# Optimization experiments

Hardware: AMD Instinct MI355X
Metric: run time of the kernel (lower is better)

## Reference

```python
import jax, jax.numpy as jnp
import numpy as np

L, D, H, KV, HD, KVL, I, PL = 8, 2048, 8, 2, 256, 4096, 8192, 256
FULL = (4,)          # layers with full (global) attention / global RoPE
POS = 2047           # current decode position (cache write slot)
N_REP = H // KV      # GQA expansion factor


def rms(x, eps=1e-6):
    # RMSNorm without scale (v_norm); scale applied by caller where needed
    return x * jax.lax.rsqrt(jnp.mean(x * x, axis=-1, keepdims=True) + eps)


def rope(x, cos, sin):
    half = HD // 2
    rot = jnp.concatenate([-x[..., half:], x[..., :half]], axis=-1)
    return x * cos + rot * sin


def _rope_tables(theta):
    inv = 1.0 / (theta ** (np.arange(0, HD, 2, dtype=np.float32) / HD))
    ang = jnp.asarray(POS * inv, dtype=jnp.float32)
    return jnp.concatenate([jnp.cos(ang)] * 2), jnp.concatenate([jnp.sin(ang)] * 2)


def setup_inputs() -> dict:
    key = jax.random.key(0)
    ks = jax.random.split(key, 24)
    r = lambda k, s, sc=0.02: jax.random.normal(k, s, jnp.float32) * sc
    gains = lambda k, s: 1.0 + jax.random.normal(k, s, jnp.float32) * 0.02
    cos_s, sin_s = _rope_tables(10000.0)
    cos_f, sin_f = _rope_tables(1000000.0)
    um = jnp.zeros((1, 1, KVL, 1), jnp.float32).at[0, 0, POS, 0].set(1.0)
    mask = jnp.where(jnp.arange(KVL) <= POS, 0.0, -1e9).astype(jnp.float32)
    return {
        "hidden_states": r(ks[0], (1, 1, D), 1.0),
        "causal_mask": mask,
        "update_mask": um,
        "per_layer_combined": r(ks[1], (1, 1, L * PL), 1.0),
        "cos_s": cos_s, "sin_s": sin_s, "cos_f": cos_f, "sin_f": sin_f,
        "K_in": r(ks[2], (L, KV, KVL, HD)),
        "V_in": r(ks[3], (L, KV, KVL, HD)),
        "w_q": r(ks[4], (L, H * HD, D)),
        "w_k": r(ks[5], (L, KV * HD, D)),
        "w_v": r(ks[6], (L, KV * HD, D)),
        "w_o": r(ks[7], (L, D, H * HD)),
        "g_in_ln": gains(ks[8], (L, D)),
        "g_q_norm": gains(ks[9], (L, HD)),
        "g_k_norm": gains(ks[10], (L, HD)),
        "g_post_attn_ln": gains(ks[11], (L, D)),
        "g_pre_ff_ln": gains(ks[12], (L, D)),
        "g_post_ff_ln": gains(ks[13], (L, D)),
        "w_gate": r(ks[14], (L, I, D)),
        "w_up": r(ks[15], (L, I, D)),
        "w_down": r(ks[16], (L, D, I)),
        "w_plg": r(ks[17], (L, PL, D)),
        "w_plp": r(ks[18], (L, D, PL)),
        "g_post_pl_ln": gains(ks[19], (L, D)),
        "layer_scalar": jnp.ones((L,), jnp.float32),
    }


def reference(hidden_states, causal_mask, update_mask, per_layer_combined,
              cos_s, sin_s, cos_f, sin_f, K_in, V_in,
              w_q, w_k, w_v, w_o,
              g_in_ln, g_q_norm, g_k_norm, g_post_attn_ln, g_pre_ff_ln, g_post_ff_ln,
              w_gate, w_up, w_down, w_plg, w_plp, g_post_pl_ln, layer_scalar):
    um = update_mask[0, 0]          # [KVL,1] one-hot at write position
    h = hidden_states[0, 0]         # [D], batch=1/seq=1 decode
    K_outs, V_outs = [], []
    for i in range(L):
        cos, sin = (cos_f, sin_f) if i in FULL else (cos_s, sin_s)
        # --- attention block ---
        res = h
        x = rms(h) * g_in_ln[i]
        q = rms((w_q[i] @ x).reshape(H, HD)) * g_q_norm[i]
        q = rope(q, cos, sin)                                   # [H,HD]
        k = rms((w_k[i] @ x).reshape(KV, HD)) * g_k_norm[i]
        k = rope(k, cos, sin)                                   # [KV,HD]
        v = rms((w_v[i] @ x).reshape(KV, HD))                    # v_norm (no scale)
        # full-tensor masked blend = KV cache write (faithful to source)
        Ko = K_in[i] * (1.0 - um) + k[:, None, :] * um          # [KV,KVL,HD]
        Vo = V_in[i] * (1.0 - um) + v[:, None, :] * um
        K_outs.append(Ko); V_outs.append(Vo)
        Ke = jnp.repeat(Ko, N_REP, axis=0)                      # GQA expand [H,KVL,HD]
        Ve = jnp.repeat(Vo, N_REP, axis=0)
        scores = jnp.einsum('hd,hkd->hk', q, Ke) + causal_mask  # no 1/sqrt(hd) in source
        attn = jax.nn.softmax(scores, axis=-1)
        ao = jnp.einsum('hk,hkd->hd', attn, Ve).reshape(H * HD)
        ao = rms(w_o[i] @ ao) * g_post_attn_ln[i]
        h = res + ao
        # --- gated MLP ---
        res = h
        xm = rms(h) * g_pre_ff_ln[i]
        m = w_down[i] @ (jax.nn.gelu(w_gate[i] @ xm, approximate=True) * (w_up[i] @ xm))
        h = res + rms(m) * g_post_ff_ln[i]
        # --- per-layer input gating ---
        res = h
        pls = per_layer_combined[0, 0, i * PL:(i + 1) * PL]     # [PL]
        g = jax.nn.gelu(w_plg[i] @ h, approximate=True) * pls
        h = res + rms(w_plp[i] @ g) * g_post_pl_ln[i]
        h = h * layer_scalar[i]
    return (h[None, None, :], jnp.stack(K_outs), jnp.stack(V_outs))
```

## Files before the change

kernel.cpp:

```cpp
#include <hip/hip_runtime.h>

#define NL   8
#define DIM  2048
#define NH   8
#define NKV  2
#define HD   256
#define KVL  4096
#define FFI  8192
#define PLD  256
#define POS  2047
#define NCH  16
#define CP   128

__device__ __forceinline__ float dot4(float4 a, float4 b){
  return a.x*b.x + a.y*b.y + a.z*b.z + a.w*b.w;
}

__device__ __forceinline__ float waveAllSum(float v){
#pragma unroll
  for(int o=1;o<64;o<<=1) v += __shfl_xor(v,o,64);
  return v;
}

__device__ __forceinline__ float waveAllMax(float v){
#pragma unroll
  for(int o=1;o<64;o<<=1) v = fmaxf(v, __shfl_xor(v,o,64));
  return v;
}

__device__ __forceinline__ float blockSum256(float v, float* red){
  int lane = threadIdx.x & 63, w = threadIdx.x >> 6;
  v = waveAllSum(v);
  __syncthreads();
  if(lane==0) red[w] = v;
  __syncthreads();
  return red[0]+red[1]+red[2]+red[3];
}

__device__ __forceinline__ float gelu_tanh(float v){
  return 0.5f*v*(1.0f + tanhf(0.7978845608028654f*(v + 0.044715f*v*v*v)));
}

__global__ __launch_bounds__(256) void qkv_k(
    const float* __restrict__ Wq, const float* __restrict__ Wk,
    const float* __restrict__ Wv,
    const float* __restrict__ hC, const float* __restrict__ u,
    const float* __restrict__ g_pl, const float* __restrict__ lsc,
    const float* __restrict__ g_in, const float* __restrict__ hidden,
    float* __restrict__ hA, float* __restrict__ qkv){
  __shared__ float xs[DIM];
  __shared__ float red[4];
  int tid = threadIdx.x;
  float hv[8];
  if(hidden){
#pragma unroll
    for(int i=0;i<8;i++) hv[i] = hidden[tid + i*256];
  } else {
    float uv[8]; float ss1 = 0.f;
#pragma unroll
    for(int i=0;i<8;i++){ uv[i] = u[tid + i*256]; ss1 += uv[i]*uv[i]; }
    ss1 = blockSum256(ss1, red);
    float r1 = rsqrtf(ss1*(1.f/DIM) + 1e-6f);
    float ls = lsc[0];
#pragma unroll
    for(int i=0;i<8;i++){
      int idx = tid + i*256;
      hv[i] = (hC[idx] + uv[i]*r1*g_pl[idx])*ls;
    }
  }
  float ss2 = 0.f;
#pragma unroll
  for(int i=0;i<8;i++) ss2 += hv[i]*hv[i];
  ss2 = blockSum256(ss2, red);
  float r2 = rsqrtf(ss2*(1.f/DIM) + 1e-6f);
#pragma unroll
  for(int i=0;i<8;i++){
    int idx = tid + i*256;
    xs[idx] = hv[i]*r2*g_in[idx];
    if(blockIdx.x==0) hA[idx] = hv[i];
  }
  __syncthreads();
  int lane = tid & 63, wv = tid >> 6;
  int r = blockIdx.x*4 + wv;
  const float* W; int row;
  if(r < 2048){ W = Wq; row = r; }
  else if(r < 2560){ W = Wk; row = r - 2048; }
  else { W = Wv; row = r - 2560; }
  const float4* Wr = (const float4*)(W + (size_t)row*DIM);
  const float4* xs4 = (const float4*)xs;
  float acc = 0.f;
#pragma unroll
  for(int i=0;i<DIM/256;i++) acc += dot4(Wr[lane + i*64], xs4[lane + i*64]);
  acc = waveAllSum(acc);
  if(lane==0) qkv[r] = acc;
}

__device__ __forceinline__ float4 normRope(const float* __restrict__ raw, int lane,
    const float* __restrict__ gain, const float* __restrict__ cosT,
    const float* __restrict__ sinT, bool doRope){
  float4 v4 = ((const float4*)raw)[lane];
  float ss = waveAllSum(dot4(v4,v4));
  float sc = rsqrtf(ss*(1.f/HD) + 1e-6f);
  float4 n;
  if(gain){
    float4 g4 = ((const float4*)gain)[lane];
    n.x=v4.x*sc*g4.x; n.y=v4.y*sc*g4.y; n.z=v4.z*sc*g4.z; n.w=v4.w*sc*g4.w;
  } else {
    n.x=v4.x*sc; n.y=v4.y*sc; n.z=v4.z*sc; n.w=v4.w*sc;
  }
  if(!doRope) return n;
  float4 np;
  np.x=__shfl_xor(n.x,32,64); np.y=__shfl_xor(n.y,32,64);
  np.z=__shfl_xor(n.z,32,64); np.w=__shfl_xor(n.w,32,64);
  float4 c4 = ((const float4*)cosT)[lane];
  float4 s4 = ((const float4*)sinT)[lane];
  float sg = (lane < 32) ? -1.f : 1.f;
  float4 o;
  o.x = n.x*c4.x + sg*np.x*s4.x;
  o.y = n.y*c4.y + sg*np.y*s4.y;
  o.z = n.z*c4.z + sg*np.z*s4.z;
  o.w = n.w*c4.w + sg*np.w*s4.w;
  return o;
}

__global__ __launch_bounds__(256) void attn_k(
    const float* __restrict__ qkv,
    const float* __restrict__ gq, const float* __restrict__ gk,
    const float* __restrict__ cosT, const float* __restrict__ sinT,
    float* __restrict__ Kc, float* __restrict__ Vc,
    float* __restrict__ pm, float* __restrict__ pl, float* __restrict__ po){
  int b = blockIdx.x;
  int tid = threadIdx.x, lane = tid & 63, wv = tid >> 6;

  if(b == NKV*NCH){
    int kvv = wv >> 1, isV = wv & 1;
    const float* raw = qkv + (isV ? 2560 : 2048) + kvv*HD;
    float4 o = normRope(raw, lane, isV ? nullptr : gk, cosT, sinT, !isV);
    float* dst = (isV ? Vc : Kc) + ((size_t)kvv*KVL + POS)*HD;
    ((float4*)dst)[lane] = o;
    return;
  }

  int kv = b >> 4, c = b & (NCH-1);
  __shared__ float q_s[4][HD];
  __shared__ float kf[HD], vf[HD];
  __shared__ float s_s[4][CP];
  __shared__ float s_w[4][CP];

  {
    float4 o = normRope(qkv + (kv*4 + wv)*HD, lane, gq, cosT, sinT, true);
    ((float4*)q_s[wv])[lane] = o;
  }
  bool fresh = (c == NCH-1);
  if(fresh){
    if(wv == 0){
      float4 o = normRope(qkv + 2048 + kv*HD, lane, gk, cosT, sinT, true);
      ((float4*)kf)[lane] = o;
    } else if(wv == 1){
      float4 o = normRope(qkv + 2560 + kv*HD, lane, nullptr, cosT, sinT, false);
      ((float4*)vf)[lane] = o;
    }
  }
  __syncthreads();

  float4 q4[4];
#pragma unroll
  for(int hh=0;hh<4;hh++) q4[hh] = ((const float4*)q_s[hh])[lane];
  const float4* Kp = (const float4*)(Kc + ((size_t)kv*KVL + c*CP)*HD);
  for(int j=0;j<CP/4;j++){
    int p = wv*(CP/4) + j;
    float4 k4 = (fresh && p==CP-1) ? ((const float4*)kf)[lane]
                                   : Kp[(size_t)p*64 + lane];
    float d0 = dot4(k4,q4[0]), d1 = dot4(k4,q4[1]);
    float d2 = dot4(k4,q4[2]), d3 = dot4(k4,q4[3]);
    d0 = waveAllSum(d0); d1 = waveAllSum(d1);
    d2 = waveAllSum(d2); d3 = waveAllSum(d3);
    if(lane==0){ s_s[0][p]=d0; s_s[1][p]=d1; s_s[2][p]=d2; s_s[3][p]=d3; }
  }
  __syncthreads();

  {
    float s0 = s_s[wv][lane], s1 = s_s[wv][lane+64];
    float m = waveAllMax(fmaxf(s0,s1));
    float e0 = __expf(s0-m), e1 = __expf(s1-m);
    s_w[wv][lane] = e0; s_w[wv][lane+64] = e1;
    float lsum = waveAllSum(e0+e1);
    if(lane==0){
      int hg = kv*4 + wv;
      pm[hg*NCH + c] = m;
      pl[hg*NCH + c] = lsum;
    }
  }
  __syncthreads();

  float acc[4] = {0.f,0.f,0.f,0.f};
  const float* Vp = Vc + ((size_t)kv*KVL + c*CP)*HD;
  for(int p=0;p<CP;p++){
    float vv = (fresh && p==CP-1) ? vf[tid] : Vp[(size_t)p*HD + tid];
#pragma unroll
    for(int hh=0;hh<4;hh++) acc[hh] += s_w[hh][p]*vv;
  }
#pragma unroll
  for(int hh=0;hh<4;hh++){
    int hg = kv*4 + hh;
    po[((size_t)hg*NCH + c)*HD + tid] = acc[hh];
  }
}

__global__ __launch_bounds__(256) void wo_k(const float* __restrict__ W,
    const float* __restrict__ pm, const float* __restrict__ pl,
    const float* __restrict__ po, float* __restrict__ y){
  __shared__ float ao_s[DIM];
  __shared__ float se_s[NH][NCH];
  __shared__ float Ms[NH];
  __shared__ float Li[NH];
  int tid = threadIdx.x;
  if(tid < NH){
    float m = -1e30f;
    for(int c=0;c<NCH;c++) m = fmaxf(m, pm[tid*NCH+c]);
    Ms[tid] = m;
  }
  __syncthreads();
  if(tid < NH*NCH){
    int h = tid >> 4, c = tid & (NCH-1);
    se_s[h][c] = __expf(pm[h*NCH+c] - Ms[h]);
  }
  __syncthreads();
  if(tid < NH){
    float L = 0.f;
    for(int c=0;c<NCH;c++) L += pl[tid*NCH+c]*se_s[tid][c];
    Li[tid] = 1.f/L;
  }
  __syncthreads();
  for(int h=0;h<NH;h++){
    float a = 0.f;
#pragma unroll
    for(int c=0;c<NCH;c++) a += po[((size_t)h*NCH+c)*HD + tid]*se_s[h][c];
    ao_s[h*HD + tid] = a*Li[h];
  }
  __syncthreads();
  int lane = tid & 63, wv = tid >> 6;
  int r = blockIdx.x*4 + wv;
  const float4* Wr = (const float4*)(W + (size_t)r*DIM);
  const float4* xs4 = (const float4*)ao_s;
  float acc = 0.f;
#pragma unroll
  for(int i=0;i<DIM/256;i++) acc += dot4(Wr[lane + i*64], xs4[lane + i*64]);
  acc = waveAllSum(acc);
  if(lane==0) y[r] = acc;
}

__global__ __launch_bounds__(256) void gateup_k(const float* __restrict__ Wg,
    const float* __restrict__ Wu, const float* __restrict__ y,
    const float* __restrict__ hA, const float* __restrict__ g_pa,
    const float* __restrict__ g_pf, float* __restrict__ hB, float* __restrict__ t){
  __shared__ float xs[DIM];
  __shared__ float red[4];
  int tid = threadIdx.x;
  float yv[8]; float ss1 = 0.f;
#pragma unroll
  for(int i=0;i<8;i++){ yv[i] = y[tid + i*256]; ss1 += yv[i]*yv[i]; }
  ss1 = blockSum256(ss1, red);
  float r1 = rsqrtf(ss1*(1.f/DIM) + 1e-6f);
  float hv[8]; float ss2 = 0.f;
#pragma unroll
  for(int i=0;i<8;i++){
    int idx = tid + i*256;
    hv[i] = hA[idx] + yv[i]*r1*g_pa[idx];
    ss2 += hv[i]*hv[i];
  }
  ss2 = blockSum256(ss2, red);
  float r2 = rsqrtf(ss2*(1.f/DIM) + 1e-6f);
#pragma unroll
  for(int i=0;i<8;i++){
    int idx = tid + i*256;
    xs[idx] = hv[i]*r2*g_pf[idx];
    if(blockIdx.x==0) hB[idx] = hv[i];
  }
  __syncthreads();
  int lane = tid & 63, wv = tid >> 6;
  int j = blockIdx.x*4 + wv;
  const float4* Gr = (const float4*)(Wg + (size_t)j*DIM);
  const float4* Ur = (const float4*)(Wu + (size_t)j*DIM);
  const float4* xs4 = (const float4*)xs;
  float ag = 0.f, au = 0.f;
#pragma unroll
  for(int i=0;i<DIM/256;i++){
    float4 bv = xs4[lane + i*64];
    ag += dot4(Gr[lane + i*64], bv);
    au += dot4(Ur[lane + i*64], bv);
  }
  ag = waveAllSum(ag);
  au = waveAllSum(au);
  if(lane==0) t[j] = gelu_tanh(ag)*au;
}

template<int C>
__global__ __launch_bounds__(256) void gemv_k(const float* __restrict__ W,
    const float* __restrict__ x, float* __restrict__ y){
  __shared__ float xs[C];
  for(int i=threadIdx.x; i<C/4; i+=256)
    ((float4*)xs)[i] = ((const float4*)x)[i];
  __syncthreads();
  int lane = threadIdx.x & 63, wv = threadIdx.x >> 6;
  int r = blockIdx.x*4 + wv;
  const float4* Wr = (const float4*)(W + (size_t)r*C);
  const float4* xs4 = (const float4*)xs;
  float acc = 0.f;
#pragma unroll
  for(int i=0;i<C/256;i++) acc += dot4(Wr[lane + i*64], xs4[lane + i*64]);
  acc = waveAllSum(acc);
  if(lane==0) y[r] = acc;
}

__global__ __launch_bounds__(256) void plg_k(const float* __restrict__ W,
    const float* __restrict__ mv, const float* __restrict__ hB,
    const float* __restrict__ g_ff, const float* __restrict__ pls,
    float* __restrict__ hCout, float* __restrict__ gb){
  __shared__ float xs[DIM];
  __shared__ float red[4];
  int tid = threadIdx.x;
  float mvv[8]; float ss1 = 0.f;
#pragma unroll
  for(int i=0;i<8;i++){ mvv[i] = mv[tid + i*256]; ss1 += mvv[i]*mvv[i]; }
  ss1 = blockSum256(ss1, red);
  float r1 = rsqrtf(ss1*(1.f/DIM) + 1e-6f);
#pragma unroll
  for(int i=0;i<8;i++){
    int idx = tid + i*256;
    float hc = hB[idx] + mvv[i]*r1*g_ff[idx];
    xs[idx] = hc;
    if(blockIdx.x==0) hCout[idx] = hc;
  }
  __syncthreads();
  int lane = tid & 63, wv = tid >> 6;
  int r = blockIdx.x*4 + wv;
  const float4* Wr = (const float4*)(W + (size_t)r*DIM);
  const float4* xs4 = (const float4*)xs;
  float acc = 0.f;
#pragma unroll
  for(int i=0;i<DIM/256;i++) acc += dot4(Wr[lane + i*64], xs4[lane + i*64]);
  acc = waveAllSum(acc);
  if(lane==0) gb[r] = gelu_tanh(acc)*pls[r];
}

__global__ __launch_bounds__(256) void final_k(const float* __restrict__ u,
    const float* __restrict__ hC, const float* __restrict__ g_pl,
    const float* __restrict__ lsc, float* __restrict__ out){
  __shared__ float red[4];
  int tid = threadIdx.x;
  float uv[8]; float ss1 = 0.f;
#pragma unroll
  for(int i=0;i<8;i++){ uv[i] = u[tid + i*256]; ss1 += uv[i]*uv[i]; }
  ss1 = blockSum256(ss1, red);
  float r1 = rsqrtf(ss1*(1.f/DIM) + 1e-6f);
  float ls = lsc[0];
#pragma unroll
  for(int i=0;i<8;i++){
    int idx = tid + i*256;
    out[idx] = (hC[idx] + uv[i]*r1*g_pl[idx])*ls;
  }
}

extern "C" void kernel_launch(void* const* d_in, const int* in_sizes, int n_in,
                              void* d_out, int out_size, void* d_ws, size_t ws_size,
                              hipStream_t stream){
  const float* hidden   = (const float*)d_in[0];
  const float* plc      = (const float*)d_in[3];
  const float* cos_s    = (const float*)d_in[4];
  const float* sin_s    = (const float*)d_in[5];
  const float* cos_f    = (const float*)d_in[6];
  const float* sin_f    = (const float*)d_in[7];
  const float* K_in     = (const float*)d_in[8];
  const float* V_in     = (const float*)d_in[9];
  const float* w_q      = (const float*)d_in[10];
  const float* w_k      = (const float*)d_in[11];
  const float* w_v      = (const float*)d_in[12];
  const float* w_o      = (const float*)d_in[13];
  const float* g_in_ln  = (const float*)d_in[14];
  const float* g_q_norm = (const float*)d_in[15];
  const float* g_k_norm = (const float*)d_in[16];
  const float* g_pa_ln  = (const float*)d_in[17];
  const float* g_pf_ln  = (const float*)d_in[18];
  const float* g_ff_ln  = (const float*)d_in[19];
  const float* w_gate   = (const float*)d_in[20];
  const float* w_up     = (const float*)d_in[21];
  const float* w_down   = (const float*)d_in[22];
  const float* w_plg    = (const float*)d_in[23];
  const float* w_plp    = (const float*)d_in[24];
  const float* g_pl_ln  = (const float*)d_in[25];
  const float* l_scal   = (const float*)d_in[26];

  float* out  = (float*)d_out;
  float* outK = out + DIM;
  float* outV = outK + (size_t)NL*NKV*KVL*HD;

  float* ws   = (float*)d_ws;
  float* hA   = ws;
  float* hB   = ws + 2048;
  float* hC   = ws + 4096;
  float* qkv  = ws + 6144;
  float* y    = ws + 9216;
  float* t    = ws + 11264;
  float* mv   = ws + 19456;
  float* gb   = ws + 21504;
  float* u    = ws + 21760;
  float* pm   = ws + 23808;
  float* pl   = ws + 23936;
  float* po   = ws + 24064;

  (void)hipMemcpyAsync(outK, K_in, (size_t)NL*NKV*KVL*HD*sizeof(float),
                       hipMemcpyDeviceToDevice, stream);
  (void)hipMemcpyAsync(outV, V_in, (size_t)NL*NKV*KVL*HD*sizeof(float),
                       hipMemcpyDeviceToDevice, stream);

  for(int l=0;l<NL;l++){
    const float* cosT = (l==4) ? cos_f : cos_s;
    const float* sinT = (l==4) ? sin_f : sin_s;
    float* Kl = outK + (size_t)l*NKV*KVL*HD;
    float* Vl = outV + (size_t)l*NKV*KVL*HD;

    qkv_k<<<768,256,0,stream>>>(
        w_q + (size_t)l*NH*HD*DIM, w_k + (size_t)l*NKV*HD*DIM,
        w_v + (size_t)l*NKV*HD*DIM,
        hC, u,
        (l>0) ? g_pl_ln + (size_t)(l-1)*DIM : g_pl_ln,
        (l>0) ? l_scal + (l-1) : l_scal,
        g_in_ln + (size_t)l*DIM,
        (l==0) ? hidden : nullptr,
        hA, qkv);

    attn_k<<<NKV*NCH+1,256,0,stream>>>(qkv, g_q_norm + l*HD, g_k_norm + l*HD,
                                       cosT, sinT, Kl, Vl, pm, pl, po);

    wo_k<<<512,256,0,stream>>>(w_o + (size_t)l*DIM*NH*HD, pm, pl, po, y);

    gateup_k<<<FFI/4,256,0,stream>>>(w_gate + (size_t)l*FFI*DIM,
                                     w_up + (size_t)l*FFI*DIM,
                                     y, hA, g_pa_ln + (size_t)l*DIM,
                                     g_pf_ln + (size_t)l*DIM, hB, t);

    gemv_k<FFI><<<512,256,0,stream>>>(w_down + (size_t)l*DIM*FFI, t, mv);

    plg_k<<<PLD/4,256,0,stream>>>(w_plg + (size_t)l*PLD*DIM, mv, hB,
                                  g_ff_ln + (size_t)l*DIM, plc + l*PLD, hC, gb);

    gemv_k<PLD><<<512,256,0,stream>>>(w_plp + (size_t)l*DIM*PLD, gb, u);
  }

  final_k<<<1,256,0,stream>>>(u, hC, g_pl_ln + (size_t)(NL-1)*DIM,
                              l_scal + (NL-1), out);
}
```

Before: 976.5 us.

## Replace per-layer kernel launches with persistent megakernel using grid barriers

Merges all per-layer kernels into one persistent kernel of 256 blocks × 512 threads, with a software grid barrier between stages. This removes roughly 57 kernel launches and their inter-kernel gaps. The KV cache copy moves from two large hipMemcpyAsync calls into the QKV stage, spread across all waves. Attention is split into 256 chunks of 8 positions with a two-level softmax merge. The design relies on all 256 blocks being co-resident and adds barrier spin costs and lower per-stage parallelism.

```diff
diff --git a/kernel.cpp b/kernel.cpp
--- a/kernel.cpp
+++ b/kernel.cpp
@@ -9,8 +9,22 @@
 #define FFI  8192
 #define PLD  256
 #define POS  2047
-#define NCH  16
-#define CP   128
+#define NCH  256
+#define CP   8
+#define NBLK 256
+#define NTHR 512
+
+struct MegaP {
+  const float *hidden, *plc, *cos_s, *sin_s, *cos_f, *sin_f;
+  const float *K_in, *V_in;
+  const float *w_q, *w_k, *w_v, *w_o;
+  const float *g_in, *g_q, *g_k, *g_pa, *g_pf, *g_ff;
+  const float *w_gate, *w_up, *w_down, *w_plg, *w_plp, *g_pl, *lsc;
+  float *out, *outK, *outV;
+  float *hA, *hB, *hC, *qkvb, *y, *t, *mv, *gb, *u;
+  float *pm, *pl, *po, *po2, *Mq, *Lq;
+  unsigned *slots, *gen;
+};
 
 __device__ __forceinline__ float dot4(float4 a, float4 b){
   return a.x*b.x + a.y*b.y + a.z*b.z + a.w*b.w;
@@ -28,71 +42,20 @@
   return v;
 }
 
-__device__ __forceinline__ float blockSum256(float v, float* red){
+__device__ __forceinline__ float blockSum512(float v, float* red){
   int lane = threadIdx.x & 63, w = threadIdx.x >> 6;
   v = waveAllSum(v);
   __syncthreads();
   if(lane==0) red[w] = v;
   __syncthreads();
-  return red[0]+red[1]+red[2]+red[3];
+  float s = 0.f;
+#pragma unroll
+  for(int i=0;i<8;i++) s += red[i];
+  return s;
 }
 
 __device__ __forceinline__ float gelu_tanh(float v){
   return 0.5f*v*(1.0f + tanhf(0.7978845608028654f*(v + 0.044715f*v*v*v)));
-}
-
-__global__ __launch_bounds__(256) void qkv_k(
-    const float* __restrict__ Wq, const float* __restrict__ Wk,
-    const float* __restrict__ Wv,
-    const float* __restrict__ hC, const float* __restrict__ u,
-    const float* __restrict__ g_pl, const float* __restrict__ lsc,
-    const float* __restrict__ g_in, const float* __restrict__ hidden,
-    float* __restrict__ hA, float* __restrict__ qkv){
-  __shared__ float xs[DIM];
-  __shared__ float red[4];
-  int tid = threadIdx.x;
-  float hv[8];
-  if(hidden){
-#pragma unroll
-    for(int i=0;i<8;i++) hv[i] = hidden[tid + i*256];
-  } else {
-    float uv[8]; float ss1 = 0.f;
-#pragma unroll
-    for(int i=0;i<8;i++){ uv[i] = u[tid + i*256]; ss1 += uv[i]*uv[i]; }
-    ss1 = blockSum256(ss1, red);
-    float r1 = rsqrtf(ss1*(1.f/DIM) + 1e-6f);
-    float ls = lsc[0];
-#pragma unroll
-    for(int i=0;i<8;i++){
-      int idx = tid + i*256;
-      hv[i] = (hC[idx] + uv[i]*r1*g_pl[idx])*ls;
-    }
-  }
-  float ss2 = 0.f;
-#pragma unroll
-  for(int i=0;i<8;i++) ss2 += hv[i]*hv[i];
-  ss2 = blockSum256(ss2, red);
-  float r2 = rsqrtf(ss2*(1.f/DIM) + 1e-6f);
-#pragma unroll
-  for(int i=0;i<8;i++){
-    int idx = tid + i*256;
-    xs[idx] = hv[i]*r2*g_in[idx];
-    if(blockIdx.x==0) hA[idx] = hv[i];
-  }
-  __syncthreads();
-  int lane = tid & 63, wv = tid >> 6;
-  int r = blockIdx.x*4 + wv;
-  const float* W; int row;
-  if(r < 2048){ W = Wq; row = r; }
-  else if(r < 2560){ W = Wk; row = r - 2048; }
-  else { W = Wv; row = r - 2560; }
-  const float4* Wr = (const float4*)(W + (size_t)row*DIM);
-  const float4* xs4 = (const float4*)xs;
-  float acc = 0.f;
-#pragma unroll
-  for(int i=0;i<DIM/256;i++) acc += dot4(Wr[lane + i*64], xs4[lane + i*64]);
-  acc = waveAllSum(acc);
-  if(lane==0) qkv[r] = acc;
 }
 
 __device__ __forceinline__ float4 normRope(const float* __restrict__ raw, int lane,
@@ -123,331 +86,411 @@
   return o;
 }
 
-__global__ __launch_bounds__(256) void attn_k(
-    const float* __restrict__ qkv,
-    const float* __restrict__ gq, const float* __restrict__ gk,
-    const float* __restrict__ cosT, const float* __restrict__ sinT,
-    float* __restrict__ Kc, float* __restrict__ Vc,
-    float* __restrict__ pm, float* __restrict__ pl, float* __restrict__ po){
-  int b = blockIdx.x;
-  int tid = threadIdx.x, lane = tid & 63, wv = tid >> 6;
-
-  if(b == NKV*NCH){
-    int kvv = wv >> 1, isV = wv & 1;
-    const float* raw = qkv + (isV ? 2560 : 2048) + kvv*HD;
-    float4 o = normRope(raw, lane, isV ? nullptr : gk, cosT, sinT, !isV);
-    float* dst = (isV ? Vc : Kc) + ((size_t)kvv*KVL + POS)*HD;
-    ((float4*)dst)[lane] = o;
-    return;
-  }
-
-  int kv = b >> 4, c = b & (NCH-1);
-  __shared__ float q_s[4][HD];
-  __shared__ float kf[HD], vf[HD];
-  __shared__ float s_s[4][CP];
-  __shared__ float s_w[4][CP];
-
-  {
-    float4 o = normRope(qkv + (kv*4 + wv)*HD, lane, gq, cosT, sinT, true);
-    ((float4*)q_s[wv])[lane] = o;
-  }
-  bool fresh = (c == NCH-1);
-  if(fresh){
-    if(wv == 0){
-      float4 o = normRope(qkv + 2048 + kv*HD, lane, gk, cosT, sinT, true);
-      ((float4*)kf)[lane] = o;
-    } else if(wv == 1){
-      float4 o = normRope(qkv + 2560 + kv*HD, lane, nullptr, cosT, sinT, false);
-      ((float4*)vf)[lane] = o;
+__device__ __forceinline__ void gridBarrier(unsigned* slots, unsigned* gen, unsigned g){
+  __syncthreads();
+  int tid = threadIdx.x, bid = blockIdx.x;
+  if(tid < 64){
+    if(tid == 0){
+      __threadfence();
+      __hip_atomic_store(&slots[bid], g, __ATOMIC_RELEASE, __HIP_MEMORY_SCOPE_AGENT);
+    }
+    if(bid == 0){
+      for(;;){
+        bool ok = true;
+#pragma unroll
+        for(int i=0;i<4;i++){
+          unsigned v = __hip_atomic_load(&slots[tid*4+i], __ATOMIC_ACQUIRE,
+                                         __HIP_MEMORY_SCOPE_AGENT);
+          ok &= (v >= g);
+        }
+        if(__all(ok)) break;
+        __builtin_amdgcn_s_sleep(1);
+      }
+      if(tid == 0)
+        __hip_atomic_store(gen, g, __ATOMIC_RELEASE, __HIP_MEMORY_SCOPE_AGENT);
+    } else if(tid == 0){
+      while(__hip_atomic_load(gen, __ATOMIC_ACQUIRE, __HIP_MEMORY_SCOPE_AGENT) < g){
+        __builtin_amdgcn_s_sleep(2);
+      }
     }
   }
   __syncthreads();
-
-  float4 q4[4];
-#pragma unroll
-  for(int hh=0;hh<4;hh++) q4[hh] = ((const float4*)q_s[hh])[lane];
-  const float4* Kp = (const float4*)(Kc + ((size_t)kv*KVL + c*CP)*HD);
-  for(int j=0;j<CP/4;j++){
-    int p = wv*(CP/4) + j;
-    float4 k4 = (fresh && p==CP-1) ? ((const float4*)kf)[lane]
-                                   : Kp[(size_t)p*64 + lane];
-    float d0 = dot4(k4,q4[0]), d1 = dot4(k4,q4[1]);
-    float d2 = dot4(k4,q4[2]), d3 = dot4(k4,q4[3]);
-    d0 = waveAllSum(d0); d1 = waveAllSum(d1);
-    d2 = waveAllSum(d2); d3 = waveAllSum(d3);
-    if(lane==0){ s_s[0][p]=d0; s_s[1][p]=d1; s_s[2][p]=d2; s_s[3][p]=d3; }
+}
+
+__global__ __launch_bounds__(NTHR, 2) void mega_k(MegaP p){
+  __shared__ float xs[FFI];
+  __shared__ float red[8];
+  float4* xs4 = (float4*)xs;
+
+  const int tid  = threadIdx.x;
+  const int bid  = blockIdx.x;
+  const int lane = tid & 63;
+  const int wv   = tid >> 6;
+  const int gw   = bid*8 + wv;
+  unsigned bgen = 0;
+
+  for(int l=0; l<NL; l++){
+    const float* Wq  = p.w_q    + (size_t)l*NH*HD*DIM;
+    const float* Wk  = p.w_k    + (size_t)l*NKV*HD*DIM;
+    const float* Wv  = p.w_v    + (size_t)l*NKV*HD*DIM;
+    const float* Wo  = p.w_o    + (size_t)l*DIM*NH*HD;
+    const float* Wg  = p.w_gate + (size_t)l*FFI*DIM;
+    const float* Wu  = p.w_up   + (size_t)l*FFI*DIM;
+    const float* Wd  = p.w_down + (size_t)l*DIM*FFI;
+    const float* Wpg = p.w_plg  + (size_t)l*PLD*DIM;
+    const float* Wpp = p.w_plp  + (size_t)l*DIM*PLD;
+    const float* cosT = (l==4) ? p.cos_f : p.cos_s;
+    const float* sinT = (l==4) ? p.sin_f : p.sin_s;
+    const float* gq = p.g_q + (size_t)l*HD;
+    const float* gk = p.g_k + (size_t)l*HD;
+    float* Kl = p.outK + (size_t)l*NKV*KVL*HD;
+    float* Vl = p.outV + (size_t)l*NKV*KVL*HD;
+    const float* Ki = p.K_in + (size_t)l*NKV*KVL*HD;
+    const float* Vi = p.V_in + (size_t)l*NKV*KVL*HD;
+
+    {
+      float hv[4];
+      if(l==0){
+#pragma unroll
+        for(int i=0;i<4;i++) hv[i] = p.hidden[tid + i*512];
+      } else {
+        const float* gpl = p.g_pl + (size_t)(l-1)*DIM;
+        float ls = p.lsc[l-1];
+        float uv[4]; float ss = 0.f;
+#pragma unroll
+        for(int i=0;i<4;i++){ uv[i] = p.u[tid + i*512]; ss += uv[i]*uv[i]; }
+        ss = blockSum512(ss, red);
+        float r1 = rsqrtf(ss*(1.f/DIM) + 1e-6f);
+#pragma unroll
+        for(int i=0;i<4;i++){
+          int idx = tid + i*512;
+          hv[i] = (p.hC[idx] + uv[i]*r1*gpl[idx])*ls;
+        }
+      }
+      float ss2 = 0.f;
+#pragma unroll
+      for(int i=0;i<4;i++) ss2 += hv[i]*hv[i];
+      ss2 = blockSum512(ss2, red);
+      float r2 = rsqrtf(ss2*(1.f/DIM) + 1e-6f);
+      const float* gin = p.g_in + (size_t)l*DIM;
+#pragma unroll
+      for(int i=0;i<4;i++){
+        int idx = tid + i*512;
+        xs[idx] = hv[i]*r2*gin[idx];
+        if(bid==0) p.hA[idx] = hv[i];
+      }
+      __syncthreads();
+
+      {
+        const float4* Wr = (const float4*)(Wq + (size_t)gw*DIM);
+        float acc = 0.f;
+#pragma unroll
+        for(int i=0;i<8;i++) acc += dot4(Wr[i*64+lane], xs4[i*64+lane]);
+        acc = waveAllSum(acc);
+        if(lane==0) p.qkvb[gw] = acc;
+      }
+      if(gw < 1024){
+        const float* W; int row;
+        if(gw < 512){ W = Wk; row = gw; } else { W = Wv; row = gw - 512; }
+        const float4* Wr = (const float4*)(W + (size_t)row*DIM);
+        float acc = 0.f;
+#pragma unroll
+        for(int i=0;i<8;i++) acc += dot4(Wr[i*64+lane], xs4[i*64+lane]);
+        acc = waveAllSum(acc);
+        if(lane==0) p.qkvb[2048 + gw] = acc;
+      }
+      {
+        int nrow, base;
+        if(gw < 1024){ nrow = 6; base = gw*6; }
+        else { nrow = 10; base = 6144 + (gw-1024)*10; }
+        for(int j2=0;j2<nrow;j2++){
+          int rr = base + j2;
+          const float4* s; float4* d;
+          if(rr < 8192){ s = (const float4*)Ki + (size_t)rr*64; d = (float4*)Kl + (size_t)rr*64; }
+          else { int r2 = rr-8192; s = (const float4*)Vi + (size_t)r2*64; d = (float4*)Vl + (size_t)r2*64; }
+          d[lane] = s[lane];
+        }
+      }
+    }
+    gridBarrier(p.slots, p.gen, ++bgen);
+
+    if(wv < 2){
+      int pair = bid*2 + wv;
+      int kv = pair & 1, c = pair >> 1;
+      float4 q4[4];
+#pragma unroll
+      for(int hh=0;hh<4;hh++)
+        q4[hh] = normRope(p.qkvb + (kv*4+hh)*HD, lane, gq, cosT, sinT, true);
+      bool last = (c == NCH-1);
+      float4 kf4 = {0,0,0,0}, vf4 = {0,0,0,0};
+      if(last){
+        kf4 = normRope(p.qkvb + 2048 + kv*HD, lane, gk, cosT, sinT, true);
+        vf4 = normRope(p.qkvb + 2560 + kv*HD, lane, nullptr, cosT, sinT, false);
+      }
+      float sc[4] = {-1e30f,-1e30f,-1e30f,-1e30f};
+      const float4* Kp = (const float4*)(Ki + (size_t)kv*KVL*HD);
+#pragma unroll
+      for(int j=0;j<CP;j++){
+        int pp = c*CP + j;
+        float4 k4 = (last && j==CP-1) ? kf4 : Kp[(size_t)pp*64 + lane];
+#pragma unroll
+        for(int hh=0;hh<4;hh++){
+          float d = waveAllSum(dot4(k4, q4[hh]));
+          if(lane==j) sc[hh] = d;
+        }
+      }
+      float e[4];
+#pragma unroll
+      for(int hh=0;hh<4;hh++){
+        float mm = sc[hh];
+#pragma unroll
+        for(int o=1;o<8;o<<=1) mm = fmaxf(mm, __shfl_xor(mm,o,64));
+        e[hh] = __expf(sc[hh]-mm);
+        float ll = e[hh];
+#pragma unroll
+        for(int o=1;o<8;o<<=1) ll += __shfl_xor(ll,o,64);
+        if(lane==0){
+          int hg = kv*4 + hh;
+          p.pm[hg*NCH + c] = mm;
+          p.pl[hg*NCH + c] = ll;
+        }
+      }
+      float4 acc4[4] = {{0,0,0,0},{0,0,0,0},{0,0,0,0},{0,0,0,0}};
+      const float4* Vp = (const float4*)(Vi + (size_t)kv*KVL*HD);
+#pragma unroll
+      for(int j=0;j<CP;j++){
+        int pp = c*CP + j;
+        float4 v4 = (last && j==CP-1) ? vf4 : Vp[(size_t)pp*64 + lane];
+#pragma unroll
+        for(int hh=0;hh<4;hh++){
+          float w = __shfl(e[hh], j, 64);
+          acc4[hh].x += w*v4.x; acc4[hh].y += w*v4.y;
+          acc4[hh].z += w*v4.z; acc4[hh].w += w*v4.w;
+        }
+      }
+#pragma unroll
+      for(int hh=0;hh<4;hh++){
+        int hg = kv*4 + hh;
+        ((float4*)p.po)[(size_t)(hg*NCH + c)*64 + lane] = acc4[hh];
+      }
+    } else if(wv == 2 && bid < 4){
+      int kvv = bid >> 1, isV = bid & 1;
+      float4 o = isV ? normRope(p.qkvb + 2560 + kvv*HD, lane, nullptr, cosT, sinT, false)
+                     : normRope(p.qkvb + 2048 + kvv*HD, lane, gk, cosT, sinT, true);
+      float* dst = (isV ? Vl : Kl) + ((size_t)kvv*KVL + POS)*HD;
+      ((float4*)dst)[lane] = o;
+    }
+    gridBarrier(p.slots, p.gen, ++bgen);
+
+    if(wv == 0 && bid < 32){
+      int h = bid >> 2, qq = bid & 3;
+      float pmv = p.pm[h*NCH + qq*64 + lane];
+      float plv = p.pl[h*NCH + qq*64 + lane];
+      float Mq = waveAllMax(pmv);
+      float e = __expf(pmv - Mq);
+      float Lq = waveAllSum(plv * e);
+      float4 acc = {0,0,0,0};
+      const float4* pp = (const float4*)p.po + (size_t)(h*NCH + qq*64)*64;
+#pragma unroll 4
+      for(int c2=0;c2<64;c2++){
+        float w = __shfl(e, c2, 64);
+        float4 v = pp[c2*64 + lane];
+        acc.x += w*v.x; acc.y += w*v.y; acc.z += w*v.z; acc.w += w*v.w;
+      }
+      ((float4*)p.po2)[(h*4+qq)*64 + lane] = acc;
+      if(lane==0){ p.Mq[h*4+qq] = Mq; p.Lq[h*4+qq] = Lq; }
+    }
+    gridBarrier(p.slots, p.gen, ++bgen);
+
+    {
+      int h = wv;
+      float m0=p.Mq[h*4+0], m1=p.Mq[h*4+1], m2=p.Mq[h*4+2], m3=p.Mq[h*4+3];
+      float M = fmaxf(fmaxf(m0,m1), fmaxf(m2,m3));
+      float s0=__expf(m0-M), s1=__expf(m1-M), s2=__expf(m2-M), s3=__expf(m3-M);
+      float L = s0*p.Lq[h*4+0] + s1*p.Lq[h*4+1] + s2*p.Lq[h*4+2] + s3*p.Lq[h*4+3];
+      const float4* q2 = (const float4*)p.po2;
+      float4 a0 = q2[(h*4+0)*64+lane], a1 = q2[(h*4+1)*64+lane];
+      float4 a2 = q2[(h*4+2)*64+lane], a3 = q2[(h*4+3)*64+lane];
+      float inv = 1.f/L;
+      float4 ao;
+      ao.x = (s0*a0.x + s1*a1.x + s2*a2.x + s3*a3.x)*inv;
+      ao.y = (s0*a0.y + s1*a1.y + s2*a2.y + s3*a3.y)*inv;
+      ao.z = (s0*a0.z + s1*a1.z + s2*a2.z + s3*a3.z)*inv;
+      ao.w = (s0*a0.w + s1*a1.w + s2*a2.w + s3*a3.w)*inv;
+      xs4[h*64 + lane] = ao;
+      __syncthreads();
+      const float4* Wr = (const float4*)(Wo + (size_t)gw*DIM);
+      float acc = 0.f;
+#pragma unroll
+      for(int i=0;i<8;i++) acc += dot4(Wr[i*64+lane], xs4[i*64+lane]);
+      acc = waveAllSum(acc);
+      if(lane==0) p.y[gw] = acc;
+    }
+    gridBarrier(p.slots, p.gen, ++bgen);
+
+    {
+      float yv[4]; float ss1 = 0.f;
+#pragma unroll
+      for(int i=0;i<4;i++){ yv[i] = p.y[tid + i*512]; ss1 += yv[i]*yv[i]; }
+      ss1 = blockSum512(ss1, red);
+      float r1 = rsqrtf(ss1*(1.f/DIM) + 1e-6f);
+      const float* gpa = p.g_pa + (size_t)l*DIM;
+      const float* gpf = p.g_pf + (size_t)l*DIM;
+      float hv[4]; float ss2 = 0.f;
+#pragma unroll
+      for(int i=0;i<4;i++){
+        int idx = tid + i*512;
+        hv[i] = p.hA[idx] + yv[i]*r1*gpa[idx];
+        ss2 += hv[i]*hv[i];
+      }
+      ss2 = blockSum512(ss2, red);
+      float r2 = rsqrtf(ss2*(1.f/DIM) + 1e-6f);
+#pragma unroll
+      for(int i=0;i<4;i++){
+        int idx = tid + i*512;
+        xs[idx] = hv[i]*r2*gpf[idx];
+        if(bid==0) p.hB[idx] = hv[i];
+      }
+      __syncthreads();
+#pragma unroll
+      for(int rr=0;rr<4;rr++){
+        int j = gw*4 + rr;
+        const float4* Gr = (const float4*)(Wg + (size_t)j*DIM);
+        const float4* Ur = (const float4*)(Wu + (size_t)j*DIM);
+        float ag = 0.f, au = 0.f;
+#pragma unroll
+        for(int i=0;i<8;i++){
+          float4 bv = xs4[i*64+lane];
+          ag += dot4(Gr[i*64+lane], bv);
+          au += dot4(Ur[i*64+lane], bv);
+        }
+        ag = waveAllSum(ag);
+        au = waveAllSum(au);
+        if(lane==0) p.t[j] = gelu_tanh(ag)*au;
+      }
+    }
+    gridBarrier(p.slots, p.gen, ++bgen);
+
+    {
+#pragma unroll
+      for(int i=0;i<4;i++) xs4[tid + i*512] = ((const float4*)p.t)[tid + i*512];
+      __syncthreads();
+      const float4* Wr = (const float4*)(Wd + (size_t)gw*FFI);
+      float acc = 0.f;
+#pragma unroll
+      for(int i=0;i<32;i++) acc += dot4(Wr[i*64+lane], xs4[i*64+lane]);
+      acc = waveAllSum(acc);
+      if(lane==0) p.mv[gw] = acc;
+    }
+    gridBarrier(p.slots, p.gen, ++bgen);
+
+    if(bid < 32){
+      float mvv[4]; float ss1 = 0.f;
+#pragma unroll
+      for(int i=0;i<4;i++){ mvv[i] = p.mv[tid + i*512]; ss1 += mvv[i]*mvv[i]; }
+      ss1 = blockSum512(ss1, red);
+      float r1 = rsqrtf(ss1*(1.f/DIM) + 1e-6f);
+      const float* gff = p.g_ff + (size_t)l*DIM;
+#pragma unroll
+      for(int i=0;i<4;i++){
+        int idx = tid + i*512;
+        float hc = p.hB[idx] + mvv[i]*r1*gff[idx];
+        xs[idx] = hc;
+        if(bid==0) p.hC[idx] = hc;
+      }
+      __syncthreads();
+      const float4* Wr = (const float4*)(Wpg + (size_t)gw*DIM);
+      float acc = 0.f;
+#pragma unroll
+      for(int i=0;i<8;i++) acc += dot4(Wr[i*64+lane], xs4[i*64+lane]);
+      acc = waveAllSum(acc);
+      if(lane==0) p.gb[gw] = gelu_tanh(acc)*p.plc[l*PLD + gw];
+    }
+    gridBarrier(p.slots, p.gen, ++bgen);
+
+    {
+      if(tid < 64) xs4[tid] = ((const float4*)p.gb)[tid];
+      __syncthreads();
+      const float4* Wr = (const float4*)(Wpp + (size_t)gw*PLD);
+      float acc = dot4(Wr[lane], xs4[lane]);
+      acc = waveAllSum(acc);
+      if(lane==0) p.u[gw] = acc;
+    }
+    gridBarrier(p.slots, p.gen, ++bgen);
   }
-  __syncthreads();
-
-  {
-    float s0 = s_s[wv][lane], s1 = s_s[wv][lane+64];
-    float m = waveAllMax(fmaxf(s0,s1));
-    float e0 = __expf(s0-m), e1 = __expf(s1-m);
-    s_w[wv][lane] = e0; s_w[wv][lane+64] = e1;
-    float lsum = waveAllSum(e0+e1);
-    if(lane==0){
-      int hg = kv*4 + wv;
-      pm[hg*NCH + c] = m;
-      pl[hg*NCH + c] = lsum;
-    }
-  }
-  __syncthreads();
-
-  float acc[4] = {0.f,0.f,0.f,0.f};
-  const float* Vp = Vc + ((size_t)kv*KVL + c*CP)*HD;
-  for(int p=0;p<CP;p++){
-    float vv = (fresh && p==CP-1) ? vf[tid] : Vp[(size_t)p*HD + tid];
-#pragma unroll
-    for(int hh=0;hh<4;hh++) acc[hh] += s_w[hh][p]*vv;
-  }
-#pragma unroll
-  for(int hh=0;hh<4;hh++){
-    int hg = kv*4 + hh;
-    po[((size_t)hg*NCH + c)*HD + tid] = acc[hh];
-  }
-}
-
-__global__ __launch_bounds__(256) void wo_k(const float* __restrict__ W,
-    const float* __restrict__ pm, const float* __restrict__ pl,
-    const float* __restrict__ po, float* __restrict__ y){
-  __shared__ float ao_s[DIM];
-  __shared__ float se_s[NH][NCH];
-  __shared__ float Ms[NH];
-  __shared__ float Li[NH];
-  int tid = threadIdx.x;
-  if(tid < NH){
-    float m = -1e30f;
-    for(int c=0;c<NCH;c++) m = fmaxf(m, pm[tid*NCH+c]);
-    Ms[tid] = m;
-  }
-  __syncthreads();
-  if(tid < NH*NCH){
-    int h = tid >> 4, c = tid & (NCH-1);
-    se_s[h][c] = __expf(pm[h*NCH+c] - Ms[h]);
-  }
-  __syncthreads();
-  if(tid < NH){
-    float L = 0.f;
-    for(int c=0;c<NCH;c++) L += pl[tid*NCH+c]*se_s[tid][c];
-    Li[tid] = 1.f/L;
-  }
-  __syncthreads();
-  for(int h=0;h<NH;h++){
-    float a = 0.f;
-#pragma unroll
-    for(int c=0;c<NCH;c++) a += po[((size_t)h*NCH+c)*HD + tid]*se_s[h][c];
-    ao_s[h*HD + tid] = a*Li[h];
-  }
-  __syncthreads();
-  int lane = tid & 63, wv = tid >> 6;
-  int r = blockIdx.x*4 + wv;
-  const float4* Wr = (const float4*)(W + (size_t)r*DIM);
-  const float4* xs4 = (const float4*)ao_s;
-  float acc = 0.f;
-#pragma unroll
-  for(int i=0;i<DIM/256;i++) acc += dot4(Wr[lane + i*64], xs4[lane + i*64]);
-  acc = waveAllSum(acc);
-  if(lane==0) y[r] = acc;
-}
-
-__global__ __launch_bounds__(256) void gateup_k(const float* __restrict__ Wg,
-    const float* __restrict__ Wu, const float* __restrict__ y,
-    const float* __restrict__ hA, const float* __restrict__ g_pa,
-    const float* __restrict__ g_pf, float* __restrict__ hB, float* __restrict__ t){
-  __shared__ float xs[DIM];
-  __shared__ float red[4];
-  int tid = threadIdx.x;
-  float yv[8]; float ss1 = 0.f;
-#pragma unroll
-  for(int i=0;i<8;i++){ yv[i] = y[tid + i*256]; ss1 += yv[i]*yv[i]; }
-  ss1 = blockSum256(ss1, red);
-  float r1 = rsqrtf(ss1*(1.f/DIM) + 1e-6f);
-  float hv[8]; float ss2 = 0.f;
-#pragma unroll
-  for(int i=0;i<8;i++){
-    int idx = tid + i*256;
-    hv[i] = hA[idx] + yv[i]*r1*g_pa[idx];
-    ss2 += hv[i]*hv[i];
-  }
-  ss2 = blockSum256(ss2, red);
-  float r2 = rsqrtf(ss2*(1.f/DIM) + 1e-6f);
-#pragma unroll
-  for(int i=0;i<8;i++){
-    int idx = tid + i*256;
-    xs[idx] = hv[i]*r2*g_pf[idx];
-    if(blockIdx.x==0) hB[idx] = hv[i];
-  }
-  __syncthreads();
-  int lane = tid & 63, wv = tid >> 6;
-  int j = blockIdx.x*4 + wv;
-  const float4* Gr = (const float4*)(Wg + (size_t)j*DIM);
-  const float4* Ur = (const float4*)(Wu + (size_t)j*DIM);
-  const float4* xs4 = (const float4*)xs;
-  float ag = 0.f, au = 0.f;
-#pragma unroll
-  for(int i=0;i<DIM/256;i++){
-    float4 bv = xs4[lane + i*64];
-    ag += dot4(Gr[lane + i*64], bv);
-    au += dot4(Ur[lane + i*64], bv);
-  }
-  ag = waveAllSum(ag);
-  au = waveAllSum(au);
-  if(lane==0) t[j] = gelu_tanh(ag)*au;
-}
-
-template<int C>
-__global__ __launch_bounds__(256) void gemv_k(const float* __restrict__ W,
-    const float* __restrict__ x, float* __restrict__ y){
-  __shared__ float xs[C];
-  for(int i=threadIdx.x; i<C/4; i+=256)
-    ((float4*)xs)[i] = ((const float4*)x)[i];
-  __syncthreads();
-  int lane = threadIdx.x & 63, wv = threadIdx.x >> 6;
-  int r = blockIdx.x*4 + wv;
-  const float4* Wr = (const float4*)(W + (size_t)r*C);
-  const float4* xs4 = (const float4*)xs;
-  float acc = 0.f;
-#pragma unroll
-  for(int i=0;i<C/256;i++) acc += dot4(Wr[lane + i*64], xs4[lane + i*64]);
-  acc = waveAllSum(acc);
-  if(lane==0) y[r] = acc;
-}
-
-__global__ __launch_bounds__(256) void plg_k(const float* __restrict__ W,
-    const float* __restrict__ mv, const float* __restrict__ hB,
-    const float* __restrict__ g_ff, const float* __restrict__ pls,
-    float* __restrict__ hCout, float* __restrict__ gb){
-  __shared__ float xs[DIM];
-  __shared__ float red[4];
-  int tid = threadIdx.x;
-  float mvv[8]; float ss1 = 0.f;
-#pragma unroll
-  for(int i=0;i<8;i++){ mvv[i] = mv[tid + i*256]; ss1 += mvv[i]*mvv[i]; }
-  ss1 = blockSum256(ss1, red);
-  float r1 = rsqrtf(ss1*(1.f/DIM) + 1e-6f);
-#pragma unroll
-  for(int i=0;i<8;i++){
-    int idx = tid + i*256;
-    float hc = hB[idx] + mvv[i]*r1*g_ff[idx];
-    xs[idx] = hc;
-    if(blockIdx.x==0) hCout[idx] = hc;
-  }
-  __syncthreads();
-  int lane = tid & 63, wv = tid >> 6;
-  int r = blockIdx.x*4 + wv;
-  const float4* Wr = (const float4*)(W + (size_t)r*DIM);
-  const float4* xs4 = (const float4*)xs;
-  float acc = 0.f;
-#pragma unroll
-  for(int i=0;i<DIM/256;i++) acc += dot4(Wr[lane + i*64], xs4[lane + i*64]);
-  acc = waveAllSum(acc);
-  if(lane==0) gb[r] = gelu_tanh(acc)*pls[r];
-}
-
-__global__ __launch_bounds__(256) void final_k(const float* __restrict__ u,
-    const float* __restrict__ hC, const float* __restrict__ g_pl,
-    const float* __restrict__ lsc, float* __restrict__ out){
-  __shared__ float red[4];
-  int tid = threadIdx.x;
-  float uv[8]; float ss1 = 0.f;
-#pragma unroll
-  for(int i=0;i<8;i++){ uv[i] = u[tid + i*256]; ss1 += uv[i]*uv[i]; }
-  ss1 = blockSum256(ss1, red);
-  float r1 = rsqrtf(ss1*(1.f/DIM) + 1e-6f);
-  float ls = lsc[0];
-#pragma unroll
-  for(int i=0;i<8;i++){
-    int idx = tid + i*256;
-    out[idx] = (hC[idx] + uv[i]*r1*g_pl[idx])*ls;
+
+  if(bid == 0){
+    float uv[4]; float ss = 0.f;
+#pragma unroll
+    for(int i=0;i<4;i++){ uv[i] = p.u[tid + i*512]; ss += uv[i]*uv[i]; }
+    ss = blockSum512(ss, red);
+    float r1 = rsqrtf(ss*(1.f/DIM) + 1e-6f);
+    float ls = p.lsc[NL-1];
+    const float* gpl = p.g_pl + (size_t)(NL-1)*DIM;
+#pragma unroll
+    for(int i=0;i<4;i++){
+      int idx = tid + i*512;
+      p.out[idx] = (p.hC[idx] + uv[i]*r1*gpl[idx])*ls;
+    }
   }
 }
 
 extern "C" void kernel_launch(void* const* d_in, const int* in_sizes, int n_in,
                               void* d_out, int out_size, void* d_ws, size_t ws_size,
                               hipStream_t stream){
-  const float* hidden   = (const float*)d_in[0];
-  const float* plc      = (const float*)d_in[3];
-  const float* cos_s    = (const float*)d_in[4];
-  const float* sin_s    = (const float*)d_in[5];
-  const float* cos_f    = (const float*)d_in[6];
-  const float* sin_f    = (const float*)d_in[7];
-  const float* K_in     = (const float*)d_in[8];
-  const float* V_in     = (const float*)d_in[9];
-  const float* w_q      = (const float*)d_in[10];
-  const float* w_k      = (const float*)d_in[11];
-  const float* w_v      = (const float*)d_in[12];
-  const float* w_o      = (const float*)d_in[13];
-  const float* g_in_ln  = (const float*)d_in[14];
-  const float* g_q_norm = (const float*)d_in[15];
-  const float* g_k_norm = (const float*)d_in[16];
-  const float* g_pa_ln  = (const float*)d_in[17];
-  const float* g_pf_ln  = (const float*)d_in[18];
-  const float* g_ff_ln  = (const float*)d_in[19];
-  const float* w_gate   = (const float*)d_in[20];
-  const float* w_up     = (const float*)d_in[21];
-  const float* w_down   = (const float*)d_in[22];
-  const float* w_plg    = (const float*)d_in[23];
-  const float* w_plp    = (const float*)d_in[24];
-  const float* g_pl_ln  = (const float*)d_in[25];
-  const float* l_scal   = (const float*)d_in[26];
-
-  float* out  = (float*)d_out;
-  float* outK = out + DIM;
-  float* outV = outK + (size_t)NL*NKV*KVL*HD;
-
-  float* ws   = (float*)d_ws;
-  float* hA   = ws;
-  float* hB   = ws + 2048;
-  float* hC   = ws + 4096;
-  float* qkv  = ws + 6144;
-  float* y    = ws + 9216;
-  float* t    = ws + 11264;
-  float* mv   = ws + 19456;
-  float* gb   = ws + 21504;
-  float* u    = ws + 21760;
-  float* pm   = ws + 23808;
-  float* pl   = ws + 23936;
-  float* po   = ws + 24064;
-
-  (void)hipMemcpyAsync(outK, K_in, (size_t)NL*NKV*KVL*HD*sizeof(float),
-                       hipMemcpyDeviceToDevice, stream);
-  (void)hipMemcpyAsync(outV, V_in, (size_t)NL*NKV*KVL*HD*sizeof(float),
-                       hipMemcpyDeviceToDevice, stream);
-
-  for(int l=0;l<NL;l++){
-    const float* cosT = (l==4) ? cos_f : cos_s;
-    const float* sinT = (l==4) ? sin_f : sin_s;
-    float* Kl = outK + (size_t)l*NKV*KVL*HD;
-    float* Vl = outV + (size_t)l*NKV*KVL*HD;
-
-    qkv_k<<<768,256,0,stream>>>(
-        w_q + (size_t)l*NH*HD*DIM, w_k + (size_t)l*NKV*HD*DIM,
-        w_v + (size_t)l*NKV*HD*DIM,
-        hC, u,
-        (l>0) ? g_pl_ln + (size_t)(l-1)*DIM : g_pl_ln,
-        (l>0) ? l_scal + (l-1) : l_scal,
-        g_in_ln + (size_t)l*DIM,
-        (l==0) ? hidden : nullptr,
-        hA, qkv);
-
-    attn_k<<<NKV*NCH+1,256,0,stream>>>(qkv, g_q_norm + l*HD, g_k_norm + l*HD,
-                                       cosT, sinT, Kl, Vl, pm, pl, po);
-
-    wo_k<<<512,256,0,stream>>>(w_o + (size_t)l*DIM*NH*HD, pm, pl, po, y);
-
-    gateup_k<<<FFI/4,256,0,stream>>>(w_gate + (size_t)l*FFI*DIM,
-                                     w_up + (size_t)l*FFI*DIM,
-                                     y, hA, g_pa_ln + (size_t)l*DIM,
-                                     g_pf_ln + (size_t)l*DIM, hB, t);
-
-    gemv_k<FFI><<<512,256,0,stream>>>(w_down + (size_t)l*DIM*FFI, t, mv);
-
-    plg_k<<<PLD/4,256,0,stream>>>(w_plg + (size_t)l*PLD*DIM, mv, hB,
-                                  g_ff_ln + (size_t)l*DIM, plc + l*PLD, hC, gb);
-
-    gemv_k<PLD><<<512,256,0,stream>>>(w_plp + (size_t)l*DIM*PLD, gb, u);
-  }
-
-  final_k<<<1,256,0,stream>>>(u, hC, g_pl_ln + (size_t)(NL-1)*DIM,
-                              l_scal + (NL-1), out);
-}
+  MegaP p;
+  p.hidden = (const float*)d_in[0];
+  p.plc    = (const float*)d_in[3];
+  p.cos_s  = (const float*)d_in[4];
+  p.sin_s  = (const float*)d_in[5];
+  p.cos_f  = (const float*)d_in[6];
+  p.sin_f  = (const float*)d_in[7];
+  p.K_in   = (const float*)d_in[8];
+  p.V_in   = (const float*)d_in[9];
+  p.w_q    = (const float*)d_in[10];
+  p.w_k    = (const float*)d_in[11];
+  p.w_v    = (const float*)d_in[12];
+  p.w_o    = (const float*)d_in[13];
+  p.g_in   = (const float*)d_in[14];
+  p.g_q    = (const float*)d_in[15];
+  p.g_k    = (const float*)d_in[16];
+  p.g_pa   = (const float*)d_in[17];
+  p.g_pf   = (const float*)d_in[18];
+  p.g_ff   = (const float*)d_in[19];
+  p.w_gate = (const float*)d_in[20];
+  p.w_up   = (const float*)d_in[21];
+  p.w_down = (const float*)d_in[22];
+  p.w_plg  = (const float*)d_in[23];
+  p.w_plp  = (const float*)d_in[24];
+  p.g_pl   = (const float*)d_in[25];
+  p.lsc    = (const float*)d_in[26];
+
+  float* out = (float*)d_out;
+  p.out  = out;
+  p.outK = out + DIM;
+  p.outV = p.outK + (size_t)NL*NKV*KVL*HD;
+
+  unsigned* bar = (unsigned*)d_ws;
+  p.slots = bar;
+  p.gen   = bar + 320;
+
+  float* fws = (float*)d_ws + 512;
+  p.hA   = fws;
+  p.hB   = fws + 2048;
+  p.hC   = fws + 4096;
+  p.qkvb = fws + 6144;
+  p.y    = fws + 9216;
+  p.t    = fws + 11264;
+  p.mv   = fws + 19456;
+  p.gb   = fws + 21504;
+  p.u    = fws + 21760;
+  p.pm   = fws + 23808;
+  p.pl   = fws + 25856;
+  p.po   = fws + 27904;
+  p.po2  = fws + 552192;
+  p.Mq   = fws + 560384;
+  p.Lq   = fws + 560416;
+
+  (void)hipMemsetAsync(d_ws, 0, 2048, stream);
+  mega_k<<<NBLK, NTHR, 0, stream>>>(p);
+}
```

Result: slower. 3.563 ms (+264.9%).
